# Performance work log

Hardware: AMD Instinct MI355X
Metric: run time of the kernel (lower is better)

## Reference

```python
import jax, jax.numpy as jnp
import numpy as np
import math

B = 8
H_GRID, W_GRID = 24, 24          # patch grid (24x24 -> 576 patches)
P = H_GRID * W_GRID              # 576
TOP_N = 3                        # TOKEN_CONFIGS[192]['top_n_per_region']
NUM_TOKENS = 336                 # Stage1_CONFIGS[192]
K = min(math.ceil(NUM_TOKENS / B), 144 * TOP_N)
DIST_THRESH = math.sqrt(280.0)   # distance=280
HEADS = 16
D = 1024
N_LAYERS_SIM = 9                 # hidden_states[16:25]


def _dist_penalty():
    # penalty(i,j) = max(0, 1 - dist2d(i,j)/threshold), shape [P, P]
    ys, xs = jnp.meshgrid(jnp.arange(H_GRID), jnp.arange(W_GRID), indexing='ij')
    coords = jnp.stack([ys, xs], axis=-1).reshape(-1, 2).astype(jnp.float32)
    diff = coords[:, None, :] - coords[None, :, :]
    dist = jnp.sqrt(jnp.sum(diff * diff, axis=-1))
    return 1.0 - jnp.minimum(dist / DIST_THRESH, 1.0)


def setup_inputs() -> dict:
    key = jax.random.key(0)
    k1, k2, k3 = jax.random.split(key, 3)
    attn = jax.random.uniform(k1, (B, HEADS, P + 1, P + 1), dtype=jnp.float32)
    hidden_agg = jax.random.normal(k2, (B, P + 1, D), dtype=jnp.float32)
    stacked_hs = jax.random.normal(k3, (N_LAYERS_SIM, B, P + 1, D), dtype=jnp.float32)
    return {"attn": attn, "hidden_agg": hidden_agg, "stacked_hs": stacked_hs}


def reference(attn, hidden_agg, stacked_hs):
    dist_penalty = _dist_penalty()                      # [P, P]

    # CLS-attention importance metric
    cls_attn = attn[:, :, 0, 1:]                        # [B, heads, P]
    metric = cls_attn.sum(axis=1)                       # [B, P]

    # region-wise (2x2 blocks) top-n selection
    m2d = metric.reshape(B, H_GRID // 2, 2, W_GRID // 2, 2)
    regions = m2d.transpose(0, 1, 3, 2, 4).reshape(B, -1, 4)   # [B, 144, 4]
    _, loc = jax.lax.top_k(regions, TOP_N)              # [B, 144, TOP_N]
    ly, lx = loc // 2, loc % 2
    rid = jnp.arange(144)
    ry, rx = rid // (W_GRID // 2), rid % (W_GRID // 2)
    gy = ry[None, :, None] * 2 + ly
    gx = rx[None, :, None] * 2 + lx
    cand = (gy * W_GRID + gx).reshape(B, -1)            # [B, 144*TOP_N]

    # global top-K over regional candidates
    cand_scores = jnp.take_along_axis(metric, cand, axis=1)
    _, top_c = jax.lax.top_k(cand_scores, K)
    bench = jnp.take_along_axis(cand, top_c, axis=1)
    bench = jnp.sort(bench, axis=1)                     # [B, K]

    # cosine similarity of layer-averaged patch tokens
    avg_hs = stacked_hs.mean(axis=0)[:, 1:, :]          # [B, P, D]
    nrm = avg_hs / jnp.maximum(jnp.linalg.norm(avg_hs, axis=-1, keepdims=True), 1e-12)
    bench_nrm = jnp.take_along_axis(nrm, bench[..., None], axis=1)  # [B, K, D]
    sim_rows = jnp.einsum('bkd,bpd->bkp', bench_nrm, nrm)           # [B, K, P]

    w = jax.nn.relu(sim_rows) * dist_penalty[bench]     # [B, K, P]
    w = w / (w.sum(axis=-1, keepdims=True) + 1e-8)
    # self weight = 1.0 (scatter_)
    b_idx = jnp.arange(B)[:, None]
    k_idx = jnp.arange(K)[None, :]
    w = w.at[b_idx, k_idx, bench].set(1.0)

    patch_agg = hidden_agg[:, 1:, :]                    # [B, P, D]
    out = jnp.einsum('bkp,bpd->bkd', w, patch_agg)      # [B, K, D]
    return out, bench
```

## Files before the change

### kernel.cpp

```cpp
#include <hip/hip_runtime.h>
#include <stdint.h>

#define B_ 8
#define HGRID 24
#define PN 576
#define PP1 577
#define HEADS 16
#define DD 1024
#define NL 9
#define KS 42
#define NREG 144
#define NCAND 432
#define DIST_THRESH_F 16.733200530681511f

__device__ __forceinline__ float dist_penalty(int q, int p) {
    float dy = (float)(q / HGRID) - (float)(p / HGRID);
    float dx = (float)(q % HGRID) - (float)(p % HGRID);
    float d = sqrtf(dy * dy + dx * dx);
    return 1.0f - fminf(d / DIST_THRESH_F, 1.0f);
}

__global__ __launch_bounds__(512) void select_kernel(const float* __restrict__ attn,
                                                     int* __restrict__ bench_out,
                                                     float* __restrict__ bench_f_out) {
    __shared__ float ms[PN];
    __shared__ int cand[NCAND];
    __shared__ unsigned long long key[512];
    __shared__ int bsort[KS];
    int b = blockIdx.x;
    int tid = threadIdx.x;
    const size_t plane = (size_t)PP1 * PP1;
    for (int p = tid; p < PN; p += 512) {
        size_t base = (size_t)b * HEADS * plane + 1 + p;
        float s = 0.f;
#pragma unroll
        for (int h = 0; h < HEADS; ++h) s += attn[base + (size_t)h * plane];
        ms[p] = s;
    }
    __syncthreads();
    if (tid < NREG) {
        int ry = tid / 12, rx = tid % 12;
        float v[4]; int pid[4];
#pragma unroll
        for (int e = 0; e < 4; ++e) {
            int gy = ry * 2 + (e >> 1), gx = rx * 2 + (e & 1);
            pid[e] = gy * HGRID + gx;
            v[e] = ms[pid[e]];
        }
        bool used[4] = {false, false, false, false};
#pragma unroll
        for (int n = 0; n < 3; ++n) {
            int best = -1; float bv = -1e30f;
#pragma unroll
            for (int e = 0; e < 4; ++e)
                if (!used[e] && v[e] > bv) { bv = v[e]; best = e; }
            used[best] = true;
            cand[tid * 3 + n] = pid[best];
        }
    }
    __syncthreads();
    if (tid < NCAND) {
        unsigned int sb = __float_as_uint(ms[cand[tid]]);
        key[tid] = ((unsigned long long)sb << 32) | (unsigned long long)(0xFFFFFFFFu - (unsigned)tid);
    } else {
        key[tid] = 0ull;
    }
    for (int size = 2; size <= 512; size <<= 1) {
        for (int stride = size >> 1; stride > 0; stride >>= 1) {
            __syncthreads();
            int partner = tid ^ stride;
            if (partner > tid) {
                bool desc = ((tid & size) == 0);
                unsigned long long a = key[tid], c = key[partner];
                if (desc ? (a < c) : (a > c)) { key[tid] = c; key[partner] = a; }
            }
        }
    }
    __syncthreads();
    if (tid < KS) {
        int orig = (int)(0xFFFFFFFFu - (unsigned int)(key[tid] & 0xFFFFFFFFull));
        bsort[tid] = cand[orig];
    }
    __syncthreads();
    if (tid == 0) {
        for (int i = 1; i < KS; ++i) {
            int x = bsort[i], j = i - 1;
            while (j >= 0 && bsort[j] > x) { bsort[j + 1] = bsort[j]; --j; }
            bsort[j + 1] = x;
        }
    }
    __syncthreads();
    if (tid < KS) {
        bench_out[b * KS + tid] = bsort[tid];
        bench_f_out[b * KS + tid] = (float)bsort[tid];
    }
}

__global__ __launch_bounds__(256) void nrm_kernel(const float* __restrict__ shs,
                                                  float* __restrict__ nrm) {
    int blk = blockIdx.x;
    int b = blk / PN, p = blk % PN;
    int t = threadIdx.x;
    const size_t lstride = (size_t)B_ * PP1 * DD;
    size_t rowbase = ((size_t)b * PP1 + (p + 1)) * DD + t * 4;
    float4 acc = make_float4(0.f, 0.f, 0.f, 0.f);
#pragma unroll
    for (int l = 0; l < NL; ++l) {
        const float4 v = *reinterpret_cast<const float4*>(shs + rowbase + (size_t)l * lstride);
        acc.x += v.x; acc.y += v.y; acc.z += v.z; acc.w += v.w;
    }
    acc.x /= 9.0f; acc.y /= 9.0f; acc.z /= 9.0f; acc.w /= 9.0f;
    float ss = acc.x * acc.x + acc.y * acc.y + acc.z * acc.z + acc.w * acc.w;
#pragma unroll
    for (int o = 32; o > 0; o >>= 1) ss += __shfl_down(ss, o, 64);
    __shared__ float wsum[4];
    int lane = t & 63, wv = t >> 6;
    if (lane == 0) wsum[wv] = ss;
    __syncthreads();
    float total = wsum[0] + wsum[1] + wsum[2] + wsum[3];
    float scale = 1.0f / fmaxf(sqrtf(total), 1e-12f);
    float4 o4 = make_float4(acc.x * scale, acc.y * scale, acc.z * scale, acc.w * scale);
    *reinterpret_cast<float4*>(nrm + ((size_t)b * PN + p) * DD + t * 4) = o4;
}

__global__ __launch_bounds__(256) void sim_kernel(const float* __restrict__ nrm,
                                                  const int* __restrict__ bench,
                                                  float* __restrict__ w) {
    __shared__ __align__(16) float As[48][68];
    __shared__ __align__(16) float Bs[32][68];
    __shared__ int bsh[KS];
    int tile = blockIdx.x;
    int b = blockIdx.y;
    int tid = threadIdx.x;
    int tm = tid >> 4, tn = tid & 15;
    int p0 = tile * 32;
    if (tid < KS) bsh[tid] = bench[b * KS + tid];
    for (int i = tid; i < 6 * 68; i += 256) As[42 + i / 68][i % 68] = 0.f;
    float acc[3][2] = {};
    const float* nb = nrm + (size_t)b * PN * DD;
    for (int c = 0; c < 16; ++c) {
        int d0 = c * 64;
        __syncthreads();
#pragma unroll
        for (int it = 0; it < 3; ++it) {
            int idx = it * 256 + tid;
            if (idx < 672) {
                int row = idx >> 4, col = (idx & 15) * 4;
                float4 v = *reinterpret_cast<const float4*>(nb + (size_t)bsh[row] * DD + d0 + col);
                *reinterpret_cast<float4*>(&As[row][col]) = v;
            }
        }
#pragma unroll
        for (int it = 0; it < 2; ++it) {
            int idx = it * 256 + tid;
            int row = idx >> 4, col = (idx & 15) * 4;
            float4 v = *reinterpret_cast<const float4*>(nb + (size_t)(p0 + row) * DD + d0 + col);
            *reinterpret_cast<float4*>(&Bs[row][col]) = v;
        }
        __syncthreads();
#pragma unroll
        for (int kk = 0; kk < 64; kk += 4) {
            float4 a0 = *reinterpret_cast<const float4*>(&As[tm * 3 + 0][kk]);
            float4 a1 = *reinterpret_cast<const float4*>(&As[tm * 3 + 1][kk]);
            float4 a2 = *reinterpret_cast<const float4*>(&As[tm * 3 + 2][kk]);
            float4 b0 = *reinterpret_cast<const float4*>(&Bs[tn * 2 + 0][kk]);
            float4 b1 = *reinterpret_cast<const float4*>(&Bs[tn * 2 + 1][kk]);
            acc[0][0] += a0.x * b0.x + a0.y * b0.y + a0.z * b0.z + a0.w * b0.w;
            acc[0][1] += a0.x * b1.x + a0.y * b1.y + a0.z * b1.z + a0.w * b1.w;
            acc[1][0] += a1.x * b0.x + a1.y * b0.y + a1.z * b0.z + a1.w * b0.w;
            acc[1][1] += a1.x * b1.x + a1.y * b1.y + a1.z * b1.z + a1.w * b1.w;
            acc[2][0] += a2.x * b0.x + a2.y * b0.y + a2.z * b0.z + a2.w * b0.w;
            acc[2][1] += a2.x * b1.x + a2.y * b1.y + a2.z * b1.z + a2.w * b1.w;
        }
    }
#pragma unroll
    for (int i = 0; i < 3; ++i) {
        int k = tm * 3 + i;
        if (k >= KS) continue;
        int q = bsh[k];
#pragma unroll
        for (int j = 0; j < 2; ++j) {
            int p = p0 + tn * 2 + j;
            float s = fmaxf(acc[i][j], 0.f) * dist_penalty(q, p);
            w[((size_t)b * KS + k) * PN + p] = s;
        }
    }
}

__global__ __launch_bounds__(256) void wnorm_kernel(float* __restrict__ w,
                                                    const int* __restrict__ bench) {
    int blk = blockIdx.x;
    float* row = w + (size_t)blk * PN;
    int t = threadIdx.x;
    float v0 = row[t], v1 = row[t + 256], v2 = (t < 64) ? row[t + 512] : 0.f;
    float s = v0 + v1 + v2;
#pragma unroll
    for (int o = 32; o > 0; o >>= 1) s += __shfl_down(s, o, 64);
    __shared__ float ws4[4];
    int lane = t & 63, wv = t >> 6;
    if (lane == 0) ws4[wv] = s;
    __syncthreads();
    float total = ws4[0] + ws4[1] + ws4[2] + ws4[3];
    float scale = 1.0f / (total + 1e-8f);
    int bp = bench[blk];
    row[t] = (t == bp) ? 1.0f : v0 * scale;
    row[t + 256] = (t + 256 == bp) ? 1.0f : v1 * scale;
    if (t < 64) row[t + 512] = (t + 512 == bp) ? 1.0f : v2 * scale;
}

__global__ __launch_bounds__(256) void out_kernel(const float* __restrict__ w,
                                                  const float* __restrict__ hidden,
                                                  float* __restrict__ out) {
    __shared__ __align__(16) float As[48][36];
    __shared__ __align__(16) float Bs[32][36];
    int ntile = blockIdx.x;
    int b = blockIdx.y;
    int tid = threadIdx.x;
    int tm = tid >> 4, tn = tid & 15;
    int n0 = ntile * 32;
    for (int i = tid; i < 6 * 36; i += 256) As[42 + i / 36][i % 36] = 0.f;
    float acc[3][2] = {};
    const float* wb = w + (size_t)b * KS * PN;
    const float* hb = hidden + ((size_t)b * PP1 + 1) * DD;
    for (int c = 0; c < 18; ++c) {
        int p0 = c * 32;
        __syncthreads();
#pragma unroll
        for (int it = 0; it < 2; ++it) {
            int idx = it * 256 + tid;
            if (idx < 336) {
                int row = idx >> 3, col = (idx & 7) * 4;
                float4 v = *reinterpret_cast<const float4*>(wb + (size_t)row * PN + p0 + col);
                *reinterpret_cast<float4*>(&As[row][col]) = v;
            }
        }
        {
            int row = tid >> 3, col = (tid & 7) * 4;
            float4 v = *reinterpret_cast<const float4*>(hb + (size_t)(p0 + row) * DD + n0 + col);
            *reinterpret_cast<float4*>(&Bs[row][col]) = v;
        }
        __syncthreads();
#pragma unroll
        for (int kk = 0; kk < 32; ++kk) {
            float a0 = As[tm * 3 + 0][kk], a1 = As[tm * 3 + 1][kk], a2 = As[tm * 3 + 2][kk];
            float b0 = Bs[kk][tn * 2 + 0], b1 = Bs[kk][tn * 2 + 1];
            acc[0][0] += a0 * b0; acc[0][1] += a0 * b1;
            acc[1][0] += a1 * b0; acc[1][1] += a1 * b1;
            acc[2][0] += a2 * b0; acc[2][1] += a2 * b1;
        }
    }
#pragma unroll
    for (int i = 0; i < 3; ++i) {
        int k = tm * 3 + i;
        if (k >= KS) continue;
#pragma unroll
        for (int j = 0; j < 2; ++j)
            out[((size_t)b * KS + k) * DD + n0 + tn * 2 + j] = acc[i][j];
    }
}

extern "C" void kernel_launch(void* const* d_in, const int* in_sizes, int n_in,
                              void* d_out, int out_size, void* d_ws, size_t ws_size,
                              hipStream_t stream) {
    const float* attn = (const float*)d_in[0];
    const float* hidden = (const float*)d_in[1];
    const float* shs = (const float*)d_in[2];
    float* out = (float*)d_out;
    float* bench_f = out + (size_t)B_ * KS * DD;

    char* ws = (char*)d_ws;
    float* nrm = (float*)ws;
    int* bench = (int*)(ws + 18874368);
    float* w = (float*)(ws + 18874368 + 1536);

    select_kernel<<<dim3(B_), dim3(512), 0, stream>>>(attn, bench, bench_f);
    nrm_kernel<<<dim3(B_ * PN), dim3(256), 0, stream>>>(shs, nrm);
    sim_kernel<<<dim3(18, B_), dim3(256), 0, stream>>>(nrm, bench, w);
    wnorm_kernel<<<dim3(B_ * KS), dim3(256), 0, stream>>>(w, bench);
    out_kernel<<<dim3(32, B_), dim3(256), 0, stream>>>(w, hidden, out);
}
```

Measured before the change: 421.0 us.

## Split-K the similarity GEMM and replace bitonic sort with rank-based selection

The similarity kernel now splits the 1024-wide reduction into four chunks across a third grid dimension and writes partial sums. The normalization kernel adds the partials and applies the relu and distance penalty there. This raises the sim kernel's block count from 144 to 576 so more compute units are busy. Separately, the top-K selection replaces the 512-element bitonic sort and the single-thread insertion sort with a parallel counting-rank selection. The cost is extra partial-sum traffic and workspace.

```diff
diff --git a/kernel.cpp b/kernel.cpp
--- a/kernel.cpp
+++ b/kernel.cpp
@@ -11,6 +11,7 @@
 #define KS 42
 #define NREG 144
 #define NCAND 432
+#define KSPLIT 4
 #define DIST_THRESH_F 16.733200530681511f
 
 __device__ __forceinline__ float dist_penalty(int q, int p) {
@@ -25,8 +26,8 @@
                                                      float* __restrict__ bench_f_out) {
     __shared__ float ms[PN];
     __shared__ int cand[NCAND];
-    __shared__ unsigned long long key[512];
-    __shared__ int bsort[KS];
+    __shared__ float csc[NCAND];
+    __shared__ int sel[KS];
     int b = blockIdx.x;
     int tid = threadIdx.x;
     const size_t plane = (size_t)PP1 * PP1;
@@ -59,40 +60,26 @@
         }
     }
     __syncthreads();
+    if (tid < NCAND) csc[tid] = ms[cand[tid]];
+    __syncthreads();
     if (tid < NCAND) {
-        unsigned int sb = __float_as_uint(ms[cand[tid]]);
-        key[tid] = ((unsigned long long)sb << 32) | (unsigned long long)(0xFFFFFFFFu - (unsigned)tid);
-    } else {
-        key[tid] = 0ull;
-    }
-    for (int size = 2; size <= 512; size <<= 1) {
-        for (int stride = size >> 1; stride > 0; stride >>= 1) {
-            __syncthreads();
-            int partner = tid ^ stride;
-            if (partner > tid) {
-                bool desc = ((tid & size) == 0);
-                unsigned long long a = key[tid], c = key[partner];
-                if (desc ? (a < c) : (a > c)) { key[tid] = c; key[partner] = a; }
-            }
-        }
+        float myv = csc[tid];
+        int rank = 0;
+#pragma unroll 8
+        for (int j = 0; j < NCAND; ++j) {
+            float vj = csc[j];
+            rank += (int)((vj > myv) || (vj == myv && j < tid));
+        }
+        if (rank < KS) sel[rank] = cand[tid];
     }
     __syncthreads();
     if (tid < KS) {
-        int orig = (int)(0xFFFFFFFFu - (unsigned int)(key[tid] & 0xFFFFFFFFull));
-        bsort[tid] = cand[orig];
-    }
-    __syncthreads();
-    if (tid == 0) {
-        for (int i = 1; i < KS; ++i) {
-            int x = bsort[i], j = i - 1;
-            while (j >= 0 && bsort[j] > x) { bsort[j + 1] = bsort[j]; --j; }
-            bsort[j + 1] = x;
-        }
-    }
-    __syncthreads();
-    if (tid < KS) {
-        bench_out[b * KS + tid] = bsort[tid];
-        bench_f_out[b * KS + tid] = (float)bsort[tid];
+        int v = sel[tid];
+        int r2 = 0;
+#pragma unroll
+        for (int j = 0; j < KS; ++j) r2 += (int)(sel[j] < v);
+        bench_out[b * KS + r2] = v;
+        bench_f_out[b * KS + r2] = (float)v;
     }
 }
 
@@ -125,12 +112,13 @@
 
 __global__ __launch_bounds__(256) void sim_kernel(const float* __restrict__ nrm,
                                                   const int* __restrict__ bench,
-                                                  float* __restrict__ w) {
+                                                  float* __restrict__ wpart) {
     __shared__ __align__(16) float As[48][68];
     __shared__ __align__(16) float Bs[32][68];
     __shared__ int bsh[KS];
     int tile = blockIdx.x;
     int b = blockIdx.y;
+    int kc = blockIdx.z;
     int tid = threadIdx.x;
     int tm = tid >> 4, tn = tid & 15;
     int p0 = tile * 32;
@@ -138,7 +126,7 @@
     for (int i = tid; i < 6 * 68; i += 256) As[42 + i / 68][i % 68] = 0.f;
     float acc[3][2] = {};
     const float* nb = nrm + (size_t)b * PN * DD;
-    for (int c = 0; c < 16; ++c) {
+    for (int c = kc * 4; c < kc * 4 + 4; ++c) {
         int d0 = c * 64;
         __syncthreads();
 #pragma unroll
@@ -173,27 +161,38 @@
             acc[2][1] += a2.x * b1.x + a2.y * b1.y + a2.z * b1.z + a2.w * b1.w;
         }
     }
+    float* wp = wpart + (size_t)kc * B_ * KS * PN;
 #pragma unroll
     for (int i = 0; i < 3; ++i) {
         int k = tm * 3 + i;
         if (k >= KS) continue;
-        int q = bsh[k];
 #pragma unroll
         for (int j = 0; j < 2; ++j) {
             int p = p0 + tn * 2 + j;
-            float s = fmaxf(acc[i][j], 0.f) * dist_penalty(q, p);
-            w[((size_t)b * KS + k) * PN + p] = s;
-        }
-    }
-}
-
-__global__ __launch_bounds__(256) void wnorm_kernel(float* __restrict__ w,
+            wp[((size_t)b * KS + k) * PN + p] = acc[i][j];
+        }
+    }
+}
+
+__global__ __launch_bounds__(256) void wnorm_kernel(const float* __restrict__ wpart,
+                                                    float* __restrict__ w,
                                                     const int* __restrict__ bench) {
     int blk = blockIdx.x;
-    float* row = w + (size_t)blk * PN;
+    int q = bench[blk];
+    const size_t kcs = (size_t)B_ * KS * PN;
+    const float* row0 = wpart + (size_t)blk * PN;
     int t = threadIdx.x;
-    float v0 = row[t], v1 = row[t + 256], v2 = (t < 64) ? row[t + 512] : 0.f;
-    float s = v0 + v1 + v2;
+    float v[3];
+    int pidx[3] = {t, t + 256, t + 512};
+#pragma unroll
+    for (int u = 0; u < 3; ++u) {
+        int p = pidx[u];
+        if (u < 2 || t < 64) {
+            float s = row0[p] + row0[p + kcs] + row0[p + 2 * kcs] + row0[p + 3 * kcs];
+            v[u] = fmaxf(s, 0.f) * dist_penalty(q, p);
+        } else v[u] = 0.f;
+    }
+    float s = v[0] + v[1] + v[2];
 #pragma unroll
     for (int o = 32; o > 0; o >>= 1) s += __shfl_down(s, o, 64);
     __shared__ float ws4[4];
@@ -202,10 +201,10 @@
     __syncthreads();
     float total = ws4[0] + ws4[1] + ws4[2] + ws4[3];
     float scale = 1.0f / (total + 1e-8f);
-    int bp = bench[blk];
-    row[t] = (t == bp) ? 1.0f : v0 * scale;
-    row[t + 256] = (t + 256 == bp) ? 1.0f : v1 * scale;
-    if (t < 64) row[t + 512] = (t + 512 == bp) ? 1.0f : v2 * scale;
+    float* orow = w + (size_t)blk * PN;
+    orow[t] = (t == q) ? 1.0f : v[0] * scale;
+    orow[t + 256] = (t + 256 == q) ? 1.0f : v[1] * scale;
+    if (t < 64) orow[t + 512] = (t + 512 == q) ? 1.0f : v[2] * scale;
 }
 
 __global__ __launch_bounds__(256) void out_kernel(const float* __restrict__ w,
@@ -271,11 +270,12 @@
     char* ws = (char*)d_ws;
     float* nrm = (float*)ws;
     int* bench = (int*)(ws + 18874368);
-    float* w = (float*)(ws + 18874368 + 1536);
+    float* wpart = (float*)(ws + 18874368 + 1536);
+    float* w = (float*)(ws + 18874368 + 1536 + 3096576);
 
     select_kernel<<<dim3(B_), dim3(512), 0, stream>>>(attn, bench, bench_f);
     nrm_kernel<<<dim3(B_ * PN), dim3(256), 0, stream>>>(shs, nrm);
-    sim_kernel<<<dim3(18, B_), dim3(256), 0, stream>>>(nrm, bench, w);
-    wnorm_kernel<<<dim3(B_ * KS), dim3(256), 0, stream>>>(w, bench);
+    sim_kernel<<<dim3(18, B_, KSPLIT), dim3(256), 0, stream>>>(nrm, bench, wpart);
+    wnorm_kernel<<<dim3(B_ * KS), dim3(256), 0, stream>>>(wpart, w, bench);
     out_kernel<<<dim3(32, B_), dim3(256), 0, stream>>>(w, hidden, out);
 }
```

Result: faster. 378.0 us (-10.2%).
